# Kernel tuning notes

Hardware: AMD Instinct MI355X
Metric: run time of the kernel (lower is better)

## Reference

```python
import jax, jax.numpy as jnp
from jax import lax
import numpy as np

TOPK = 100
SCALE = 4.0
EXCEPT_THRESH = 0.01

B, C, H, W = 16, 80, 256, 256


def setup_inputs() -> dict:
    key = jax.random.key(0)
    k1, k2, k3 = jax.random.split(key, 3)
    heatmap = jax.random.uniform(k1, (B, C, H, W), dtype=jnp.float32)
    offset = jax.random.normal(k2, (B, 2, H, W), dtype=jnp.float32)
    wh = jax.random.uniform(k3, (B, 2, H, W), dtype=jnp.float32)
    return {"heatmap": heatmap, "offset": offset, "wh": wh}


def reference(heatmap, offset, wh):
    b, c, h, w = heatmap.shape
    # 3x3 max-pool NMS: keep only local peaks
    pooled = lax.reduce_window(heatmap, -jnp.inf, lax.max,
                               (1, 1, 3, 3), (1, 1, 1, 1), "SAME")
    keep = (pooled == heatmap).astype(heatmap.dtype)
    hm = keep * heatmap
    # top-k over all classes x spatial positions
    flat = hm.reshape(b, -1)                      # [B, C*H*W]
    scores, indices = lax.top_k(flat, TOPK)       # [B, K]
    scores = scores[:, :, None]                   # [B, K, 1]
    ids = (indices // (h * w)).astype(jnp.float32)[:, :, None]
    spatial = indices % (h * w)                   # [B, K] flat spatial index
    topk_ys = (spatial // w).astype(jnp.float32)
    topk_xs = (spatial % w).astype(jnp.float32)
    # gather offset / wh at peak locations
    off = offset.transpose(0, 2, 3, 1).reshape(b, -1, 2)   # [B, H*W, 2]
    whr = wh.transpose(0, 2, 3, 1).reshape(b, -1, 2)       # [B, H*W, 2]
    off_g = jnp.take_along_axis(off, spatial[:, :, None], axis=1)  # [B, K, 2]
    wh_g = jnp.take_along_axis(whr, spatial[:, :, None], axis=1)   # [B, K, 2]
    cx = topk_xs + off_g[:, :, 0]
    cy = topk_ys + off_g[:, :, 1]
    half_w = wh_g[:, :, 0] * 0.5
    half_h = wh_g[:, :, 1] * 0.5
    bboxes = jnp.stack([cx - half_w, cy - half_h, cx + half_w, cy + half_h], axis=-1)  # [B, K, 4]
    # mask out low-score detections with -1
    mask = scores > EXCEPT_THRESH                 # [B, K, 1]
    neg1 = jnp.float32(-1.0)
    ids = jnp.where(mask, ids, neg1)
    scores = jnp.where(mask, scores, neg1)
    bboxes = jnp.where(mask, bboxes, neg1)
    return ids, scores, bboxes * SCALE
```

## Files before the change

### kernel.cpp

```cpp
#include <hip/hip_runtime.h>
#include <stdint.h>

#define HB 16
#define HC 80
#define HH 256
#define HWD 256
#define PLANE (HH * HWD)
#define NPLANES (HB * HC)
#define K_TOP 100
#define CAP 2048
#define OUTCAP 256
#define NEG_INF (-3.402823466e38f)

__device__ __forceinline__ int blockReduceSum(int v, int* sred) {
    for (int off = 32; off > 0; off >>= 1) v += __shfl_down(v, off);
    int t = threadIdx.x;
    __syncthreads();
    if ((t & 63) == 0) sred[t >> 6] = v;
    __syncthreads();
    return sred[0] + sred[1] + sred[2] + sred[3];
}

__device__ __forceinline__ bool better(float a, int ai, float b, int bi) {
    return (a > b) || (a == b && ai < bi);
}

__device__ void bitonic256(float* sv, int* si) {
    int t = threadIdx.x;
    for (unsigned k = 2; k <= 256; k <<= 1) {
        for (unsigned j = k >> 1; j > 0; j >>= 1) {
            __syncthreads();
            unsigned i = (unsigned)t, x = i ^ j;
            if (x > i) {
                float a = sv[i], bv = sv[x];
                int ai = si[i], bi = si[x];
                bool sw = ((i & k) == 0) ? better(bv, bi, a, ai) : better(a, ai, bv, bi);
                if (sw) { sv[i] = bv; si[i] = bi; sv[x] = a; si[x] = ai; }
            }
        }
    }
    __syncthreads();
}

__global__ __launch_bounds__(256) void k_plane_topk(const float* __restrict__ heat,
                                                    float* __restrict__ wsv,
                                                    int* __restrict__ wsi) {
    int plane = blockIdx.x;
    int c = plane % HC;
    const float* pl = heat + (size_t)plane * PLANE;
    int t = threadIdx.x;

    __shared__ float rb[3][HWD + 2];
    __shared__ float bufv[CAP];
    __shared__ int   bufi[CAP];
    __shared__ float outv[OUTCAP];
    __shared__ int   outi[OUTCAP];
    __shared__ int   cnt, cnt2;
    __shared__ int   sred[4];

    if (t < 3) { rb[t][0] = NEG_INF; rb[t][HWD + 1] = NEG_INF; }

    float thr = 0.98f;
    int n = 0;
    for (int attempt = 0; attempt < 3; ++attempt) {
        if (t == 0) cnt = 0;
        __syncthreads();
        rb[0][t + 1] = pl[t];
        __syncthreads();
        float h0 = fmaxf(fmaxf(rb[0][t], rb[0][t + 1]), rb[0][t + 2]);
        float v0 = rb[0][t + 1];
        float hm1 = NEG_INF;
        for (int r = 0; r < HH; ++r) {
            int rn = r + 1;
            float h1 = NEG_INF, v1 = 0.0f;
            if (rn < HH) {
                __syncthreads();
                rb[rn % 3][t + 1] = pl[rn * HWD + t];
                __syncthreads();
                const float* rbn = rb[rn % 3];
                h1 = fmaxf(fmaxf(rbn[t], rbn[t + 1]), rbn[t + 2]);
                v1 = rbn[t + 1];
            }
            float pooled = fmaxf(fmaxf(hm1, h0), h1);
            if (v0 >= pooled && v0 > thr) {
                int p = atomicAdd(&cnt, 1);
                if (p < CAP) { bufv[p] = v0; bufi[p] = (c << 16) | (r << 8) | t; }
            }
            hm1 = h0; h0 = h1; v0 = v1;
        }
        __syncthreads();
        n = cnt;
        __syncthreads();
        if (n >= K_TOP && n <= CAP) break;
        if (n > CAP) thr = 1.0f - (1.0f - thr) * 0.25f;
        else thr = (attempt == 0) ? 0.5f : 0.01f;
    }
    int nn = min(n, CAP);

    float regv[CAP / 256];
#pragma unroll
    for (int k = 0; k < CAP / 256; ++k) {
        int s = t + (k << 8);
        regv[k] = (s < nn) ? bufv[s] : NEG_INF;
    }

    float T100;
    if (nn >= K_TOP) {
        unsigned lo = 0u, hi = 0x7f800000u;
        while (hi - lo > 1u) {
            unsigned mid = (lo + hi) >> 1u;
            float mv = __uint_as_float(mid);
            int cl = 0;
#pragma unroll
            for (int k = 0; k < CAP / 256; ++k) cl += (regv[k] >= mv) ? 1 : 0;
            int tot = blockReduceSum(cl, sred);
            if (tot >= K_TOP) lo = mid; else hi = mid;
        }
        T100 = __uint_as_float(lo);
    } else {
        T100 = NEG_INF;
    }

    outv[t] = NEG_INF; outi[t] = 0x7fffffff;
    if (t == 0) cnt2 = 0;
    __syncthreads();
#pragma unroll
    for (int k = 0; k < CAP / 256; ++k) {
        int s = t + (k << 8);
        if (s < nn && bufv[s] >= T100) {
            int p = atomicAdd(&cnt2, 1);
            if (p < OUTCAP) { outv[p] = bufv[s]; outi[p] = bufi[s]; }
        }
    }
    __syncthreads();
    int c2 = cnt2;
    if (c2 > K_TOP) bitonic256(outv, outi);
    __syncthreads();
    if (t < K_TOP) {
        wsv[plane * K_TOP + t] = outv[t];
        wsi[plane * K_TOP + t] = outi[t];
    }
}

__global__ __launch_bounds__(256) void k_batch_out(const float* __restrict__ wsv,
                                                   const int* __restrict__ wsi,
                                                   const float* __restrict__ offset,
                                                   const float* __restrict__ wh,
                                                   float* __restrict__ out) {
    int b = blockIdx.x;
    int t = threadIdx.x;
    const int NCAND = HC * K_TOP;
    const float* v_in = wsv + b * NCAND;
    const int*   i_in = wsi + b * NCAND;

    __shared__ float outv[OUTCAP];
    __shared__ int   outi[OUTCAP];
    __shared__ int   cnt2;
    __shared__ int   sred[4];

    float regv[32];
#pragma unroll
    for (int k = 0; k < 32; ++k) {
        int s = t + (k << 8);
        regv[k] = (s < NCAND) ? v_in[s] : NEG_INF;
    }
    int cl0 = 0;
#pragma unroll
    for (int k = 0; k < 32; ++k) cl0 += (regv[k] > NEG_INF) ? 1 : 0;
    int nreal = blockReduceSum(cl0, sred);

    float T100;
    if (nreal >= K_TOP) {
        unsigned lo = 0u, hi = 0x7f800000u;
        while (hi - lo > 1u) {
            unsigned mid = (lo + hi) >> 1u;
            float mv = __uint_as_float(mid);
            int cl = 0;
#pragma unroll
            for (int k = 0; k < 32; ++k) cl += (regv[k] >= mv) ? 1 : 0;
            int tot = blockReduceSum(cl, sred);
            if (tot >= K_TOP) lo = mid; else hi = mid;
        }
        T100 = __uint_as_float(lo);
    } else {
        T100 = NEG_INF;
    }

    outv[t] = NEG_INF; outi[t] = 0x7fffffff;
    if (t == 0) cnt2 = 0;
    __syncthreads();
#pragma unroll
    for (int k = 0; k < 32; ++k) {
        int s = t + (k << 8);
        if (s < NCAND && regv[k] >= T100 && regv[k] > NEG_INF) {
            int p = atomicAdd(&cnt2, 1);
            if (p < OUTCAP) { outv[p] = regv[k]; outi[p] = i_in[s]; }
        }
    }
    __syncthreads();
    bitonic256(outv, outi);

    if (t < K_TOP) {
        float val = outv[t];
        int idx = outi[t];
        bool valid = val > 0.01f;
        int cch = idx >> 16;
        int spatial = idx & 0xFFFF;
        int y = spatial >> 8, x = spatial & 0xFF;
        const float* offb = offset + (size_t)b * 2 * PLANE;
        const float* whb  = wh     + (size_t)b * 2 * PLANE;
        float o0 = offb[spatial], o1 = offb[PLANE + spatial];
        float w0 = whb[spatial],  w1 = whb[PLANE + spatial];
        float cx = (float)x + o0, cy = (float)y + o1;
        float hw = w0 * 0.5f, hh = w1 * 0.5f;
        int g = b * K_TOP + t;
        out[g]                = valid ? (float)cch : -1.0f;
        out[HB * K_TOP + g]   = valid ? val        : -1.0f;
        float b0 = valid ? (cx - hw) : -1.0f;
        float b1 = valid ? (cy - hh) : -1.0f;
        float b2 = valid ? (cx + hw) : -1.0f;
        float b3 = valid ? (cy + hh) : -1.0f;
        float* bb = out + 2 * HB * K_TOP + 4 * g;
        bb[0] = b0 * 4.0f; bb[1] = b1 * 4.0f; bb[2] = b2 * 4.0f; bb[3] = b3 * 4.0f;
    }
}

extern "C" void kernel_launch(void* const* d_in, const int* in_sizes, int n_in,
                              void* d_out, int out_size, void* d_ws, size_t ws_size,
                              hipStream_t stream) {
    (void)in_sizes; (void)n_in; (void)out_size; (void)ws_size;
    const float* heat   = (const float*)d_in[0];
    const float* offset = (const float*)d_in[1];
    const float* wh     = (const float*)d_in[2];
    float* out = (float*)d_out;
    float* wsv = (float*)d_ws;
    int*   wsi = (int*)((char*)d_ws + (size_t)NPLANES * K_TOP * sizeof(float));

    k_plane_topk<<<NPLANES, 256, 0, stream>>>(heat, wsv, wsi);
    k_batch_out<<<HB, 256, 0, stream>>>(wsv, wsi, offset, wh, out);
}
```

Baseline: 602.7 us.

## Split plane rows across wavefronts with float4 loads and shuffle-based horizontal max

The per-plane NMS scan is restructured so that each of the four wavefronts handles a 64-row strip. Each lane loads float4 chunks straight from global memory, and the horizontal 3-wide max uses wave shuffles instead of shared-memory row buffers. This removes the two block-wide barriers per row and the shared-memory staging, and it widens the loads. The cost is that halo rows are loaded twice at strip boundaries, and the atomic append order into the candidate buffer changes.

Measured after the change: 509.3 us. -15.5%, faster.

```diff
diff --git a/kernel.cpp b/kernel.cpp
--- a/kernel.cpp
+++ b/kernel.cpp
@@ -42,6 +42,26 @@
     __syncthreads();
 }
 
+__device__ __forceinline__ float4 loadrow(const float* __restrict__ pl, int r, int lane) {
+    int rc = min(max(r, 0), HH - 1);
+    float4 v = ((const float4*)(pl + rc * HWD))[lane];
+    if (r != rc) { v.x = NEG_INF; v.y = NEG_INF; v.z = NEG_INF; v.w = NEG_INF; }
+    return v;
+}
+
+__device__ __forceinline__ float4 hmax4(float4 v, int lane) {
+    float vl = __shfl_up(v.w, 1);
+    float vr = __shfl_down(v.x, 1);
+    if (lane == 0) vl = NEG_INF;
+    if (lane == 63) vr = NEG_INF;
+    float4 h;
+    h.x = fmaxf(fmaxf(vl, v.x), v.y);
+    h.y = fmaxf(fmaxf(v.x, v.y), v.z);
+    h.z = fmaxf(fmaxf(v.y, v.z), v.w);
+    h.w = fmaxf(fmaxf(v.z, v.w), vr);
+    return h;
+}
+
 __global__ __launch_bounds__(256) void k_plane_topk(const float* __restrict__ heat,
                                                     float* __restrict__ wsv,
                                                     int* __restrict__ wsi) {
@@ -49,8 +69,9 @@
     int c = plane % HC;
     const float* pl = heat + (size_t)plane * PLANE;
     int t = threadIdx.x;
-
-    __shared__ float rb[3][HWD + 2];
+    int lane = t & 63;
+    int rs = (t >> 6) << 6;
+
     __shared__ float bufv[CAP];
     __shared__ int   bufi[CAP];
     __shared__ float outv[OUTCAP];
@@ -58,35 +79,51 @@
     __shared__ int   cnt, cnt2;
     __shared__ int   sred[4];
 
-    if (t < 3) { rb[t][0] = NEG_INF; rb[t][HWD + 1] = NEG_INF; }
-
     float thr = 0.98f;
     int n = 0;
     for (int attempt = 0; attempt < 3; ++attempt) {
         if (t == 0) cnt = 0;
         __syncthreads();
-        rb[0][t + 1] = pl[t];
-        __syncthreads();
-        float h0 = fmaxf(fmaxf(rb[0][t], rb[0][t + 1]), rb[0][t + 2]);
-        float v0 = rb[0][t + 1];
-        float hm1 = NEG_INF;
-        for (int r = 0; r < HH; ++r) {
-            int rn = r + 1;
-            float h1 = NEG_INF, v1 = 0.0f;
-            if (rn < HH) {
-                __syncthreads();
-                rb[rn % 3][t + 1] = pl[rn * HWD + t];
-                __syncthreads();
-                const float* rbn = rb[rn % 3];
-                h1 = fmaxf(fmaxf(rbn[t], rbn[t + 1]), rbn[t + 2]);
-                v1 = rbn[t + 1];
+
+        float4 rm1 = loadrow(pl, rs - 1, lane);
+        float4 r0  = loadrow(pl, rs, lane);
+        float4 hA = hmax4(rm1, lane);
+        float4 hB = hmax4(r0, lane);
+        float4 vB = r0;
+
+        for (int i = 0; i < 64; i += 4) {
+            float4 n0 = loadrow(pl, rs + i + 1, lane);
+            float4 n1 = loadrow(pl, rs + i + 2, lane);
+            float4 n2 = loadrow(pl, rs + i + 3, lane);
+            float4 n3 = loadrow(pl, rs + i + 4, lane);
+#pragma unroll
+            for (int u = 0; u < 4; ++u) {
+                float4 nr = (u == 0) ? n0 : (u == 1) ? n1 : (u == 2) ? n2 : n3;
+                int row = rs + i + u;
+                float4 hC = hmax4(nr, lane);
+                float p0 = fmaxf(fmaxf(hA.x, hB.x), hC.x);
+                float p1 = fmaxf(fmaxf(hA.y, hB.y), hC.y);
+                float p2 = fmaxf(fmaxf(hA.z, hB.z), hC.z);
+                float p3 = fmaxf(fmaxf(hA.w, hB.w), hC.w);
+                int colb = lane << 2;
+                if (vB.x >= p0 && vB.x > thr) {
+                    int p = atomicAdd(&cnt, 1);
+                    if (p < CAP) { bufv[p] = vB.x; bufi[p] = (c << 16) | (row << 8) | colb; }
+                }
+                if (vB.y >= p1 && vB.y > thr) {
+                    int p = atomicAdd(&cnt, 1);
+                    if (p < CAP) { bufv[p] = vB.y; bufi[p] = (c << 16) | (row << 8) | (colb + 1); }
+                }
+                if (vB.z >= p2 && vB.z > thr) {
+                    int p = atomicAdd(&cnt, 1);
+                    if (p < CAP) { bufv[p] = vB.z; bufi[p] = (c << 16) | (row << 8) | (colb + 2); }
+                }
+                if (vB.w >= p3 && vB.w > thr) {
+                    int p = atomicAdd(&cnt, 1);
+                    if (p < CAP) { bufv[p] = vB.w; bufi[p] = (c << 16) | (row << 8) | (colb + 3); }
+                }
+                hA = hB; hB = hC; vB = nr;
             }
-            float pooled = fmaxf(fmaxf(hm1, h0), h1);
-            if (v0 >= pooled && v0 > thr) {
-                int p = atomicAdd(&cnt, 1);
-                if (p < CAP) { bufv[p] = v0; bufi[p] = (c << 16) | (r << 8) | t; }
-            }
-            hm1 = h0; h0 = h1; v0 = v1;
         }
         __syncthreads();
         n = cnt;
```
